# Performance work log

Hardware: AMD Instinct MI355X
Metric: run time of the kernel (lower is better)

## Reference

```python
import jax, jax.numpy as jnp
import numpy as np

N_NODES = 50000
N_EDGES = 640000
IN_C, HID_C, OUT_C = 64, 128, 64


def _glorot(key, fan_in, fan_out):
    lim = float(np.sqrt(6.0 / (fan_in + fan_out)))
    return jax.random.uniform(key, (fan_in, fan_out), jnp.float32, -lim, lim)


def setup_inputs() -> dict:
    key = jax.random.key(0)
    ks = jax.random.split(key, 16)
    x = jax.random.normal(ks[0], (N_NODES, IN_C), jnp.float32)
    edge_index = jax.random.randint(ks[1], (2, N_EDGES), 0, N_NODES, jnp.int64)
    # SAGEConv params: out = mean_aggr(x_j) @ Wl + x @ Wr + b
    dims = [(IN_C, HID_C), (HID_C, HID_C), (HID_C, OUT_C)]
    params = {}
    for i, (fi, fo) in enumerate(dims):
        params[f"Wl{i}"] = _glorot(ks[2 + 3 * i], fi, fo)
        params[f"Wr{i}"] = _glorot(ks[3 + 3 * i], fi, fo)
        params[f"b{i}"] = jnp.zeros((fo,), jnp.float32)
    # classifier: Linear(64,32) -> ReLU -> Linear(32,1) -> Sigmoid (dropout off in eval)
    params["Wc1"] = _glorot(ks[11], OUT_C, 32)
    params["bc1"] = jnp.zeros((32,), jnp.float32)
    params["Wc2"] = _glorot(ks[12], 32, 1)
    params["bc2"] = jnp.zeros((1,), jnp.float32)
    return {"x": x, "edge_index": edge_index, **params}


def _sage_conv(x, src, dst, Wl, Wr, b):
    # gather neighbor (source) features along edges, mean-aggregate at target
    msgs = x[src]                                                    # [E, C]
    agg = jax.ops.segment_sum(msgs, dst, num_segments=N_NODES)      # [N, C]
    deg = jax.ops.segment_sum(jnp.ones((src.shape[0], 1), x.dtype), dst,
                              num_segments=N_NODES)                 # [N, 1]
    agg = agg / jnp.maximum(deg, 1.0)
    return agg @ Wl + x @ Wr + b


def reference(x, edge_index, Wl0, Wr0, b0, Wl1, Wr1, b1, Wl2, Wr2, b2,
              Wc1, bc1, Wc2, bc2):
    src, dst = edge_index[0], edge_index[1]
    h = jax.nn.relu(_sage_conv(x, src, dst, Wl0, Wr0, b0))
    h = jax.nn.relu(_sage_conv(h, src, dst, Wl1, Wr1, b1))
    h = _sage_conv(h, src, dst, Wl2, Wr2, b2)                       # [N, 64]
    h = jax.nn.relu(h @ Wc1 + bc1)                                  # [N, 32]
    return jax.nn.sigmoid(h @ Wc2 + bc2)                            # [N, 1]
```

## Files before the change

### kernel.cpp

```cpp
#include <hip/hip_runtime.h>
#include <math.h>

#define NN 50000
#define NE 640000
#define CAP 64
#define NSTRIP (NN / 16)

typedef short short8 __attribute__((ext_vector_type(8)));
typedef float f32x4  __attribute__((ext_vector_type(4)));

__device__ __forceinline__ unsigned bfr(float f) {
    unsigned u = __float_as_uint(f);
    return (u + 0x7FFFu + ((u >> 16) & 1u)) >> 16;
}
__device__ __forceinline__ unsigned pk2(float a, float b) { return bfr(a) | (bfr(b) << 16); }
__device__ __forceinline__ float bflo(unsigned u) { return __uint_as_float(u << 16); }
__device__ __forceinline__ float bfhi(unsigned u) { return __uint_as_float(u & 0xFFFF0000u); }

__device__ __forceinline__ void packOne(const float* Wl, const float* Wr,
                                        unsigned short* wp, int idx,
                                        int CIN, int COUT) {
    int k = idx / COUT, n = idx % COUT;
    float v = (k < CIN) ? Wl[k * COUT + n] : Wr[(k - CIN) * COUT + n];
    int kt = k >> 5, quad = (k >> 3) & 3, j = k & 7;
    int nt = n >> 4, l16 = n & 15;
    int NT = COUT / 16;
    wp[(((kt * NT + nt) * 64) + quad * 16 + l16) * 8 + j] = (unsigned short)bfr(v);
}

__global__ __launch_bounds__(256) void
k_prep(const int* __restrict__ src, const int* __restrict__ dst,
       int* __restrict__ cnt, int* __restrict__ nbr,
       const float* __restrict__ x, unsigned* __restrict__ xb,
       const float* Wl0, const float* Wr0, const float* Wl1, const float* Wr1,
       const float* Wl2, const float* Wr2, const float* Wc1,
       unsigned short* wp0, unsigned short* wp1, unsigned short* wp2,
       unsigned short* wpc) {
    const int b = blockIdx.x, t = threadIdx.x;
    if (b < 2500) {
        int e = b * 256 + t;
        if (e < NE) {
            int d = dst[e];
            int p = atomicAdd(&cnt[d], 1);
            if (p < CAP) nbr[d * CAP + p] = src[e];
        }
    } else if (b < 5625) {
        int i = (b - 2500) * 256 + t;
        if (i < NN * 16) {
            float4 v = ((const float4*)x)[i];
            ((uint2*)xb)[i] = make_uint2(pk2(v.x, v.y), pk2(v.z, v.w));
        }
    } else {
        int idx = (b - 5625) * 256 + t;
        if (idx < 16384) packOne(Wl0, Wr0, wp0, idx, 64, 128);
        else if (idx < 49152) packOne(Wl1, Wr1, wp1, idx - 16384, 128, 128);
        else if (idx < 65536) packOne(Wl2, Wr2, wp2, idx - 49152, 128, 64);
        else if (idx < 67584) packOne(Wc1, Wc1, wpc, idx - 65536, 64, 32);
    }
}

template <int CIN, int RP>
__device__ __forceinline__ void
gather16(short* __restrict__ aw, const unsigned* __restrict__ xu,
         const int* __restrict__ nbr, const int* __restrict__ cnt,
         int row_base, int lane, int qw, int l16) {
    constexpr int RU = CIN / 2;
    constexpr int PC = CIN / 32;

    int dcur = cnt[row_base];
    int scur = nbr[row_base * CAP + lane];

    for (int it = 0; it < 16; ++it) {
        const int deg = dcur;
        const int sl  = scur;
        if (it + 1 < 16) {
            dcur = cnt[row_base + it + 1];
            scur = nbr[(row_base + it + 1) * CAP + lane];
        }
        const int m = (deg < CAP) ? deg : CAP;
        const int sc = (lane < m) ? sl : 0;

        float a[2 * PC] = {};
#pragma unroll 4
        for (int j = 0; j < m; j += 4) {
            const int n = __shfl(sc, (j + qw) & 63);
            const bool valid = (j + qw) < m;
            if (PC == 2) {
                const uint2 u = *(const uint2*)(xu + (size_t)n * RU + l16 * 2);
                if (valid) {
                    a[0] += bflo(u.x); a[1] += bfhi(u.x);
                    a[2] += bflo(u.y); a[3] += bfhi(u.y);
                }
            } else {
                const uint4 u = *(const uint4*)(xu + (size_t)n * RU + l16 * 4);
                if (valid) {
                    a[0] += bflo(u.x); a[1] += bfhi(u.x);
                    a[2] += bflo(u.y); a[3] += bfhi(u.y);
                    a[4] += bflo(u.z); a[5] += bfhi(u.z);
                    a[6] += bflo(u.w); a[7] += bfhi(u.w);
                }
            }
        }

#pragma unroll
        for (int c = 0; c < 2 * PC; ++c) {
            a[c] += __shfl_xor(a[c], 16);
            a[c] += __shfl_xor(a[c], 32);
        }

        if (qw == 0) {
            const float di = 1.0f / (float)((deg > 1) ? deg : 1);
            if (PC == 2) {
                uint2 o = make_uint2(pk2(a[0] * di, a[1] * di), pk2(a[2] * di, a[3] * di));
                *(uint2*)&aw[it * RP + l16 * 4] = o;
            } else {
                uint4 o = make_uint4(pk2(a[0] * di, a[1] * di), pk2(a[2] * di, a[3] * di),
                                     pk2(a[4] * di, a[5] * di), pk2(a[6] * di, a[7] * di));
                *(uint4*)&aw[it * RP + l16 * 8] = o;
            }
        }
    }
}

template <int CIN, int COUT, bool RELU>
__global__ __launch_bounds__(256) void
k_layer(const unsigned short* __restrict__ Xprev, const int* __restrict__ nbr,
        const int* __restrict__ cnt, const unsigned short* __restrict__ Wpack,
        const float* __restrict__ bias, unsigned short* __restrict__ outp) {
    constexpr int KT = (2 * CIN) / 32;
    constexpr int NT = COUT / 16;
    constexpr int RP = CIN + 8;

    __shared__ __align__(16) short As[4 * 16 * RP];

    const int t = threadIdx.x, wave = t >> 6, lane = t & 63;
    const int qw = lane >> 4, l16 = lane & 15;
    const int strip = blockIdx.x * 4 + wave;
    if (strip >= NSTRIP) return;
    const int row_base = strip * 16;

    short* aw = As + wave * 16 * RP;

    gather16<CIN, RP>(aw, (const unsigned*)Xprev, nbr, cnt, row_base, lane, qw, l16);

    f32x4 acc[NT] = {};

    for (int kt = 0; kt < KT; ++kt) {
        short8 a0;
        if (kt < KT / 2) {
            a0 = *(const short8*)&aw[l16 * RP + kt * 32 + qw * 8];
        } else {
            const int kb = kt * 32 - CIN;
            a0 = *(const short8*)(Xprev + (size_t)(row_base + l16) * CIN + kb + qw * 8);
        }
#pragma unroll
        for (int nt = 0; nt < NT; ++nt) {
            const short8 bfrag = *(const short8*)(Wpack + (size_t)((kt * NT + nt) * 64 + lane) * 8);
            acc[nt] = __builtin_amdgcn_mfma_f32_16x16x32_bf16(a0, bfrag, acc[nt], 0, 0, 0);
        }
    }

#pragma unroll
    for (int nt = 0; nt < NT; ++nt) {
        const int col = nt * 16 + l16;
        const float bb = bias[col];
#pragma unroll
        for (int rg = 0; rg < 4; ++rg) {
            const int row = row_base + qw * 4 + rg;
            float v = acc[nt][rg] + bb;
            if (RELU) v = fmaxf(v, 0.f);
            outp[(size_t)row * COUT + col] = (unsigned short)bfr(v);
        }
    }
}

__global__ __launch_bounds__(256) void
k_layer_cls(const unsigned short* __restrict__ Xprev, const int* __restrict__ nbr,
            const int* __restrict__ cnt, const unsigned short* __restrict__ Wpack,
            const unsigned short* __restrict__ WpackC, const float* __restrict__ bias,
            const float* __restrict__ bc1, const float* __restrict__ Wc2,
            const float* __restrict__ bc2, float* __restrict__ out) {
    constexpr int CIN = 128, NT = 4, KT = 8;
    constexpr int RP = CIN + 8;
    constexpr int HP = 72;

    __shared__ __align__(16) short As[4 * 16 * RP];
    __shared__ __align__(16) short Hs[4 * 16 * HP];

    const int t = threadIdx.x, wave = t >> 6, lane = t & 63;
    const int qw = lane >> 4, l16 = lane & 15;
    const int strip = blockIdx.x * 4 + wave;
    if (strip >= NSTRIP) return;
    const int row_base = strip * 16;

    short* aw = As + wave * 16 * RP;
    short* hw = Hs + wave * 16 * HP;

    gather16<CIN, RP>(aw, (const unsigned*)Xprev, nbr, cnt, row_base, lane, qw, l16);

    f32x4 acc[NT] = {};

    for (int kt = 0; kt < KT; ++kt) {
        short8 a0;
        if (kt < KT / 2) {
            a0 = *(const short8*)&aw[l16 * RP + kt * 32 + qw * 8];
        } else {
            const int kb = kt * 32 - CIN;
            a0 = *(const short8*)(Xprev + (size_t)(row_base + l16) * CIN + kb + qw * 8);
        }
#pragma unroll
        for (int nt = 0; nt < NT; ++nt) {
            const short8 bfrag = *(const short8*)(Wpack + (size_t)((kt * NT + nt) * 64 + lane) * 8);
            acc[nt] = __builtin_amdgcn_mfma_f32_16x16x32_bf16(a0, bfrag, acc[nt], 0, 0, 0);
        }
    }

#pragma unroll
    for (int nt = 0; nt < NT; ++nt) {
        const float bb = bias[nt * 16 + l16];
#pragma unroll
        for (int rg = 0; rg < 4; ++rg)
            hw[(qw * 4 + rg) * HP + nt * 16 + l16] =
                (unsigned short)bfr(acc[nt][rg] + bb);
    }

    f32x4 sacc[2] = {};
#pragma unroll
    for (int kt2 = 0; kt2 < 2; ++kt2) {
        const short8 af = *(const short8*)&hw[l16 * HP + kt2 * 32 + qw * 8];
#pragma unroll
        for (int nt2 = 0; nt2 < 2; ++nt2) {
            const short8 bf = *(const short8*)(WpackC + (size_t)((kt2 * 2 + nt2) * 64 + lane) * 8);
            sacc[nt2] = __builtin_amdgcn_mfma_f32_16x16x32_bf16(af, bf, sacc[nt2], 0, 0, 0);
        }
    }

    const float b1a = bc1[l16], b1b = bc1[16 + l16];
    const float w2a = Wc2[l16], w2b = Wc2[16 + l16];
    const float b2v = bc2[0];
#pragma unroll
    for (int rg = 0; rg < 4; ++rg) {
        float p = fmaxf(sacc[0][rg] + b1a, 0.f) * w2a +
                  fmaxf(sacc[1][rg] + b1b, 0.f) * w2b;
#pragma unroll
        for (int off = 1; off < 16; off <<= 1) p += __shfl_xor(p, off);
        if (l16 == 0) {
            const int row = row_base + qw * 4 + rg;
            out[row] = 1.0f / (1.0f + expf(-(p + b2v)));
        }
    }
}

extern "C" void kernel_launch(void* const* d_in, const int* in_sizes, int n_in,
                              void* d_out, int out_size, void* d_ws, size_t ws_size,
                              hipStream_t stream) {
    const float* x   = (const float*)d_in[0];
    const int*   ei  = (const int*)d_in[1];
    const int*   src = ei;
    const int*   dst = ei + NE;
    const float* Wl0 = (const float*)d_in[2];
    const float* Wr0 = (const float*)d_in[3];
    const float* b0  = (const float*)d_in[4];
    const float* Wl1 = (const float*)d_in[5];
    const float* Wr1 = (const float*)d_in[6];
    const float* b1  = (const float*)d_in[7];
    const float* Wl2 = (const float*)d_in[8];
    const float* Wr2 = (const float*)d_in[9];
    const float* b2  = (const float*)d_in[10];
    const float* Wc1 = (const float*)d_in[11];
    const float* bc1 = (const float*)d_in[12];
    const float* Wc2 = (const float*)d_in[13];
    const float* bc2 = (const float*)d_in[14];
    float* out = (float*)d_out;

    char*  ws   = (char*)d_ws;
    int*   cnt  = (int*)(ws);
    unsigned short* wp0 = (unsigned short*)(ws + (size_t)256 * 1024);
    unsigned short* wp1 = (unsigned short*)(ws + (size_t)352 * 1024);
    unsigned short* wp2 = (unsigned short*)(ws + (size_t)448 * 1024);
    unsigned short* wpc = (unsigned short*)(ws + (size_t)512 * 1024);
    int*   nbr  = (int*)(ws + (size_t)1 * (1 << 20));
    unsigned short* xb  = (unsigned short*)(ws + (size_t)16 * (1 << 20));
    unsigned short* h0b = (unsigned short*)(ws + (size_t)24 * (1 << 20));
    unsigned short* h1b = (unsigned short*)(ws + (size_t)40 * (1 << 20));

    const int B = 256;
    const int LAYER_GRID = (NSTRIP + 3) / 4;

    hipMemsetAsync(cnt, 0, (size_t)NN * sizeof(int), stream);
    k_prep<<<5889, B, 0, stream>>>(src, dst, cnt, nbr, x, (unsigned*)xb,
                                   Wl0, Wr0, Wl1, Wr1, Wl2, Wr2, Wc1,
                                   wp0, wp1, wp2, wpc);

    k_layer<64, 128, true><<<LAYER_GRID, B, 0, stream>>>(xb, nbr, cnt, wp0, b0, h0b);
    k_layer<128, 128, true><<<LAYER_GRID, B, 0, stream>>>(h0b, nbr, cnt, wp1, b1, h1b);
    k_layer_cls<<<LAYER_GRID, B, 0, stream>>>(h1b, nbr, cnt, wp2, wpc, b2, bc1, Wc2, bc2,
                                              out);
}
```

Baseline: 243.8 us.

## Split each 16-row strip across two waves for gather and output columns

Each 16-node strip is now handled by two waves: each wave gathers and mean-aggregates 8 of the rows into shared memory, then after a block barrier each computes half of the output column tiles with MFMA. Blocks grow to 512 threads, which doubles the number of waves working on the latency-bound neighbour gather. In exchange it adds block-wide syncs, loads the A fragments twice, and in the classifier kernel only half the waves run the final small MLP. Out-of-range strips are clamped to the last strip rather than returning early, so the barriers stay uniform across the block.

After: 241.6 us. Within noise of the previous version (-0.9%).

```diff
diff --git a/kernel.cpp b/kernel.cpp
--- a/kernel.cpp
+++ b/kernel.cpp
@@ -61,21 +61,21 @@
 
 template <int CIN, int RP>
 __device__ __forceinline__ void
-gather16(short* __restrict__ aw, const unsigned* __restrict__ xu,
-         const int* __restrict__ nbr, const int* __restrict__ cnt,
-         int row_base, int lane, int qw, int l16) {
+gather8(short* __restrict__ aw, const unsigned* __restrict__ xu,
+        const int* __restrict__ nbr, const int* __restrict__ cnt,
+        int node0, int lds_row0, int lane, int qw, int l16) {
     constexpr int RU = CIN / 2;
     constexpr int PC = CIN / 32;
 
-    int dcur = cnt[row_base];
-    int scur = nbr[row_base * CAP + lane];
-
-    for (int it = 0; it < 16; ++it) {
+    int dcur = cnt[node0];
+    int scur = nbr[node0 * CAP + lane];
+
+    for (int it = 0; it < 8; ++it) {
         const int deg = dcur;
         const int sl  = scur;
-        if (it + 1 < 16) {
-            dcur = cnt[row_base + it + 1];
-            scur = nbr[(row_base + it + 1) * CAP + lane];
+        if (it + 1 < 8) {
+            dcur = cnt[node0 + it + 1];
+            scur = nbr[(node0 + it + 1) * CAP + lane];
         }
         const int m = (deg < CAP) ? deg : CAP;
         const int sc = (lane < m) ? sl : 0;
@@ -110,40 +110,46 @@
 
         if (qw == 0) {
             const float di = 1.0f / (float)((deg > 1) ? deg : 1);
+            const int r = lds_row0 + it;
             if (PC == 2) {
                 uint2 o = make_uint2(pk2(a[0] * di, a[1] * di), pk2(a[2] * di, a[3] * di));
-                *(uint2*)&aw[it * RP + l16 * 4] = o;
+                *(uint2*)&aw[r * RP + l16 * 4] = o;
             } else {
                 uint4 o = make_uint4(pk2(a[0] * di, a[1] * di), pk2(a[2] * di, a[3] * di),
                                      pk2(a[4] * di, a[5] * di), pk2(a[6] * di, a[7] * di));
-                *(uint4*)&aw[it * RP + l16 * 8] = o;
+                *(uint4*)&aw[r * RP + l16 * 8] = o;
             }
         }
     }
 }
 
 template <int CIN, int COUT, bool RELU>
-__global__ __launch_bounds__(256) void
+__global__ __launch_bounds__(512) void
 k_layer(const unsigned short* __restrict__ Xprev, const int* __restrict__ nbr,
         const int* __restrict__ cnt, const unsigned short* __restrict__ Wpack,
         const float* __restrict__ bias, unsigned short* __restrict__ outp) {
-    constexpr int KT = (2 * CIN) / 32;
-    constexpr int NT = COUT / 16;
-    constexpr int RP = CIN + 8;
+    constexpr int KT  = (2 * CIN) / 32;
+    constexpr int NT  = COUT / 16;
+    constexpr int NTH = NT / 2;
+    constexpr int RP  = CIN + 8;
 
     __shared__ __align__(16) short As[4 * 16 * RP];
 
     const int t = threadIdx.x, wave = t >> 6, lane = t & 63;
     const int qw = lane >> 4, l16 = lane & 15;
-    const int strip = blockIdx.x * 4 + wave;
-    if (strip >= NSTRIP) return;
+    const int sl = wave >> 1;
+    const int hf = wave & 1;
+    int strip = blockIdx.x * 4 + sl;
+    if (strip >= NSTRIP) strip = NSTRIP - 1;
     const int row_base = strip * 16;
 
-    short* aw = As + wave * 16 * RP;
-
-    gather16<CIN, RP>(aw, (const unsigned*)Xprev, nbr, cnt, row_base, lane, qw, l16);
-
-    f32x4 acc[NT] = {};
+    short* aw = As + sl * 16 * RP;
+
+    gather8<CIN, RP>(aw, (const unsigned*)Xprev, nbr, cnt,
+                     row_base + hf * 8, hf * 8, lane, qw, l16);
+    __syncthreads();
+
+    f32x4 acc[NTH] = {};
 
     for (int kt = 0; kt < KT; ++kt) {
         short8 a0;
@@ -154,33 +160,34 @@
             a0 = *(const short8*)(Xprev + (size_t)(row_base + l16) * CIN + kb + qw * 8);
         }
 #pragma unroll
-        for (int nt = 0; nt < NT; ++nt) {
+        for (int ntl = 0; ntl < NTH; ++ntl) {
+            const int nt = hf * NTH + ntl;
             const short8 bfrag = *(const short8*)(Wpack + (size_t)((kt * NT + nt) * 64 + lane) * 8);
-            acc[nt] = __builtin_amdgcn_mfma_f32_16x16x32_bf16(a0, bfrag, acc[nt], 0, 0, 0);
-        }
-    }
-
-#pragma unroll
-    for (int nt = 0; nt < NT; ++nt) {
-        const int col = nt * 16 + l16;
+            acc[ntl] = __builtin_amdgcn_mfma_f32_16x16x32_bf16(a0, bfrag, acc[ntl], 0, 0, 0);
+        }
+    }
+
+#pragma unroll
+    for (int ntl = 0; ntl < NTH; ++ntl) {
+        const int col = (hf * NTH + ntl) * 16 + l16;
         const float bb = bias[col];
 #pragma unroll
         for (int rg = 0; rg < 4; ++rg) {
             const int row = row_base + qw * 4 + rg;
-            float v = acc[nt][rg] + bb;
+            float v = acc[ntl][rg] + bb;
             if (RELU) v = fmaxf(v, 0.f);
             outp[(size_t)row * COUT + col] = (unsigned short)bfr(v);
         }
     }
 }
 
-__global__ __launch_bounds__(256) void
+__global__ __launch_bounds__(512) void
 k_layer_cls(const unsigned short* __restrict__ Xprev, const int* __restrict__ nbr,
             const int* __restrict__ cnt, const unsigned short* __restrict__ Wpack,
             const unsigned short* __restrict__ WpackC, const float* __restrict__ bias,
             const float* __restrict__ bc1, const float* __restrict__ Wc2,
             const float* __restrict__ bc2, float* __restrict__ out) {
-    constexpr int CIN = 128, NT = 4, KT = 8;
+    constexpr int CIN = 128, NT = 4, KT = 8, NTH = 2;
     constexpr int RP = CIN + 8;
     constexpr int HP = 72;
 
@@ -189,16 +196,20 @@
 
     const int t = threadIdx.x, wave = t >> 6, lane = t & 63;
     const int qw = lane >> 4, l16 = lane & 15;
-    const int strip = blockIdx.x * 4 + wave;
-    if (strip >= NSTRIP) return;
+    const int sl = wave >> 1;
+    const int hf = wave & 1;
+    int strip = blockIdx.x * 4 + sl;
+    if (strip >= NSTRIP) strip = NSTRIP - 1;
     const int row_base = strip * 16;
 
-    short* aw = As + wave * 16 * RP;
-    short* hw = Hs + wave * 16 * HP;
-
-    gather16<CIN, RP>(aw, (const unsigned*)Xprev, nbr, cnt, row_base, lane, qw, l16);
-
-    f32x4 acc[NT] = {};
+    short* aw = As + sl * 16 * RP;
+    short* hw = Hs + sl * 16 * HP;
+
+    gather8<CIN, RP>(aw, (const unsigned*)Xprev, nbr, cnt,
+                     row_base + hf * 8, hf * 8, lane, qw, l16);
+    __syncthreads();
+
+    f32x4 acc[NTH] = {};
 
     for (int kt = 0; kt < KT; ++kt) {
         short8 a0;
@@ -209,44 +220,48 @@
             a0 = *(const short8*)(Xprev + (size_t)(row_base + l16) * CIN + kb + qw * 8);
         }
 #pragma unroll
-        for (int nt = 0; nt < NT; ++nt) {
+        for (int ntl = 0; ntl < NTH; ++ntl) {
+            const int nt = hf * NTH + ntl;
             const short8 bfrag = *(const short8*)(Wpack + (size_t)((kt * NT + nt) * 64 + lane) * 8);
-            acc[nt] = __builtin_amdgcn_mfma_f32_16x16x32_bf16(a0, bfrag, acc[nt], 0, 0, 0);
-        }
-    }
-
-#pragma unroll
-    for (int nt = 0; nt < NT; ++nt) {
-        const float bb = bias[nt * 16 + l16];
+            acc[ntl] = __builtin_amdgcn_mfma_f32_16x16x32_bf16(a0, bfrag, acc[ntl], 0, 0, 0);
+        }
+    }
+
+#pragma unroll
+    for (int ntl = 0; ntl < NTH; ++ntl) {
+        const int col = (hf * NTH + ntl) * 16 + l16;
+        const float bb = bias[col];
 #pragma unroll
         for (int rg = 0; rg < 4; ++rg)
-            hw[(qw * 4 + rg) * HP + nt * 16 + l16] =
-                (unsigned short)bfr(acc[nt][rg] + bb);
-    }
-
-    f32x4 sacc[2] = {};
-#pragma unroll
-    for (int kt2 = 0; kt2 < 2; ++kt2) {
-        const short8 af = *(const short8*)&hw[l16 * HP + kt2 * 32 + qw * 8];
-#pragma unroll
-        for (int nt2 = 0; nt2 < 2; ++nt2) {
-            const short8 bf = *(const short8*)(WpackC + (size_t)((kt2 * 2 + nt2) * 64 + lane) * 8);
-            sacc[nt2] = __builtin_amdgcn_mfma_f32_16x16x32_bf16(af, bf, sacc[nt2], 0, 0, 0);
-        }
-    }
-
-    const float b1a = bc1[l16], b1b = bc1[16 + l16];
-    const float w2a = Wc2[l16], w2b = Wc2[16 + l16];
-    const float b2v = bc2[0];
-#pragma unroll
-    for (int rg = 0; rg < 4; ++rg) {
-        float p = fmaxf(sacc[0][rg] + b1a, 0.f) * w2a +
-                  fmaxf(sacc[1][rg] + b1b, 0.f) * w2b;
-#pragma unroll
-        for (int off = 1; off < 16; off <<= 1) p += __shfl_xor(p, off);
-        if (l16 == 0) {
-            const int row = row_base + qw * 4 + rg;
-            out[row] = 1.0f / (1.0f + expf(-(p + b2v)));
+            hw[(qw * 4 + rg) * HP + col] = (unsigned short)bfr(acc[ntl][rg] + bb);
+    }
+    __syncthreads();
+
+    if (hf == 0) {
+        f32x4 sacc[2] = {};
+#pragma unroll
+        for (int kt2 = 0; kt2 < 2; ++kt2) {
+            const short8 af = *(const short8*)&hw[l16 * HP + kt2 * 32 + qw * 8];
+#pragma unroll
+            for (int nt2 = 0; nt2 < 2; ++nt2) {
+                const short8 bf = *(const short8*)(WpackC + (size_t)((kt2 * 2 + nt2) * 64 + lane) * 8);
+                sacc[nt2] = __builtin_amdgcn_mfma_f32_16x16x32_bf16(af, bf, sacc[nt2], 0, 0, 0);
+            }
+        }
+
+        const float b1a = bc1[l16], b1b = bc1[16 + l16];
+        const float w2a = Wc2[l16], w2b = Wc2[16 + l16];
+        const float b2v = bc2[0];
+#pragma unroll
+        for (int rg = 0; rg < 4; ++rg) {
+            float p = fmaxf(sacc[0][rg] + b1a, 0.f) * w2a +
+                      fmaxf(sacc[1][rg] + b1b, 0.f) * w2b;
+#pragma unroll
+            for (int off = 1; off < 16; off <<= 1) p += __shfl_xor(p, off);
+            if (l16 == 0) {
+                const int row = row_base + qw * 4 + rg;
+                out[row] = 1.0f / (1.0f + expf(-(p + b2v)));
+            }
         }
     }
 }
@@ -284,16 +299,15 @@
     unsigned short* h0b = (unsigned short*)(ws + (size_t)24 * (1 << 20));
     unsigned short* h1b = (unsigned short*)(ws + (size_t)40 * (1 << 20));
 
-    const int B = 256;
     const int LAYER_GRID = (NSTRIP + 3) / 4;
 
     hipMemsetAsync(cnt, 0, (size_t)NN * sizeof(int), stream);
-    k_prep<<<5889, B, 0, stream>>>(src, dst, cnt, nbr, x, (unsigned*)xb,
-                                   Wl0, Wr0, Wl1, Wr1, Wl2, Wr2, Wc1,
-                                   wp0, wp1, wp2, wpc);
-
-    k_layer<64, 128, true><<<LAYER_GRID, B, 0, stream>>>(xb, nbr, cnt, wp0, b0, h0b);
-    k_layer<128, 128, true><<<LAYER_GRID, B, 0, stream>>>(h0b, nbr, cnt, wp1, b1, h1b);
-    k_layer_cls<<<LAYER_GRID, B, 0, stream>>>(h1b, nbr, cnt, wp2, wpc, b2, bc1, Wc2, bc2,
-                                              out);
-}
+    k_prep<<<5889, 256, 0, stream>>>(src, dst, cnt, nbr, x, (unsigned*)xb,
+                                     Wl0, Wr0, Wl1, Wr1, Wl2, Wr2, Wc1,
+                                     wp0, wp1, wp2, wpc);
+
+    k_layer<64, 128, true><<<LAYER_GRID, 512, 0, stream>>>(xb, nbr, cnt, wp0, b0, h0b);
+    k_layer<128, 128, true><<<LAYER_GRID, 512, 0, stream>>>(h0b, nbr, cnt, wp1, b1, h1b);
+    k_layer_cls<<<LAYER_GRID, 512, 0, stream>>>(h1b, nbr, cnt, wp2, wpc, b2, bc1, Wc2, bc2,
+                                                out);
+}
```
